# Performance work log

Hardware: AMD Instinct MI355X
Metric: run time of the kernel (lower is better)

The kernel has to match this reference:

```python
import jax, jax.numpy as jnp
import numpy as np

NB, NWAY, NBASE, FEAT, SEM = 8, 16, 8000, 512, 300
TEMP = float(np.sqrt(FEAT))  # d_k = feat_dim // n_head = 512


def setup_inputs() -> dict:
    key = jax.random.key(0)
    ks = jax.random.split(key, 18)
    n = jax.random.normal
    s_q = float(np.sqrt(2.0 / (FEAT + FEAT)))   # std for w_qs/w_ks/w_vs (d_model + d_k)
    s_sem = float(np.sqrt(2.0 / 600.0))
    s_lin = float(np.sqrt(1.0 / 300.0))
    return {
        "support_feat": n(ks[0], (NB, NWAY, FEAT), jnp.float32),
        "base_weights": n(ks[1], (NB, NBASE, FEAT), jnp.float32),
        "support_seman": n(ks[2], (NB, NWAY, SEM), jnp.float32),
        "base_seman": n(ks[3], (NB, NBASE, SEM), jnp.float32),
        # map_sem: Linear(300,300) -> LeakyReLU(0.1) -> Linear(300,300); weights stored (in,out)
        "map_w1": n(ks[4], (SEM, SEM), jnp.float32) * s_lin,
        "map_b1": jnp.zeros((SEM,), jnp.float32),
        "map_w2": n(ks[5], (SEM, SEM), jnp.float32) * s_lin,
        "map_b2": jnp.zeros((SEM,), jnp.float32),
        # task fusion gates: Linear(feat+300 -> feat) and Linear(feat+300 -> 300)
        "visfuse_w": n(ks[6], (FEAT + SEM, FEAT), jnp.float32) * s_lin,
        "visfuse_b": jnp.zeros((FEAT,), jnp.float32),
        "semfuse_w": n(ks[7], (FEAT + SEM, SEM), jnp.float32) * s_lin,
        "semfuse_b": jnp.zeros((SEM,), jnp.float32),
        # MHA projections (bias-free), stored (in,out)
        "w_qs": n(ks[8], (FEAT, FEAT), jnp.float32) * s_q,
        "w_ks": n(ks[9], (FEAT, FEAT), jnp.float32) * s_q,
        "w_vs": n(ks[10], (FEAT, FEAT), jnp.float32) * s_q,
        "w_qs_sem": n(ks[11], (SEM, FEAT), jnp.float32) * s_sem,
        "w_ks_sem": n(ks[12], (SEM, FEAT), jnp.float32) * s_sem,
        "fc_w": n(ks[13], (FEAT, FEAT), jnp.float32) * s_q,
    }


def _map_sem(x, w1, b1, w2, b2):
    return jax.nn.leaky_relu(x @ w1 + b1, negative_slope=0.1) @ w2 + b2


def _forward(support_feat, base_weights, support_seman, base_seman,
             map_w1, map_b1, map_w2, map_b2,
             visfuse_w, visfuse_b, semfuse_w, semfuse_b,
             w_qs, w_ks, w_vs, w_qs_sem, w_ks_sem, fc_w):
    # semantic calibration of both support and base semantics (base_seman_calib=True)
    support_seman = _map_sem(support_seman, map_w1, b1=map_b1, w2=map_w2, b2=map_b2)  # (nb,nway,300)
    base_seman = _map_sem(base_seman, map_w1, b1=map_b1, w2=map_w2, b2=map_b2)        # (nb,N,300)

    # avg_task_mem over base classes (repeat over nway is a no-op for the mean)
    avg = jnp.concatenate([jnp.mean(base_weights, axis=1, keepdims=True),
                           jnp.mean(base_seman, axis=1, keepdims=True)], axis=-1)      # (nb,1,feat+300)
    gate_vis = jax.nn.sigmoid(avg @ visfuse_w + visfuse_b) + 1.0                       # (nb,1,feat)
    gate_sem = jax.nn.sigmoid(avg @ semfuse_w + semfuse_b) + 1.0                       # (nb,1,300)

    base_mem_vis = base_weights                 # un-gated value memory (v)
    k_vis = base_weights * gate_vis             # gated keys
    k_sem = base_seman * gate_sem               # gated semantic keys

    # projections (n_head=1, d_k=d_v=feat)
    q = support_feat @ w_qs                     # (nb,nway,feat)
    k = k_vis @ w_ks                            # (nb,N,feat)
    v = base_mem_vis @ w_vs                     # (nb,N,feat)
    q_tot = q + support_seman @ w_qs_sem        # semantic-fused q
    k_tot = k + k_sem @ w_ks_sem                # semantic-fused k

    # each support sample attends over the shared base memory of its episode
    attn_score = jnp.einsum('bwd,bnd->bwn', q_tot, k_tot) / TEMP                       # (nb,nway,N)
    attn = jax.nn.softmax(attn_score, axis=-1)
    out = jnp.einsum('bwn,bnd->bwd', attn, v) @ fc_w + support_feat                    # residual
    # SupportCalibrator returns (support_center, support_attn=attn_score)
    return out, attn_score


def reference(support_feat, base_weights, support_seman, base_seman,
              map_w1, map_b1, map_w2, map_b2,
              visfuse_w, visfuse_b, semfuse_w, semfuse_b,
              w_qs, w_ks, w_vs, w_qs_sem, w_ks_sem, fc_w):
    return _forward(support_feat, base_weights, support_seman, base_seman,
                    map_w1, map_b1, map_w2, map_b2,
                    visfuse_w, visfuse_b, semfuse_w, semfuse_b,
                    w_qs, w_ks, w_vs, w_qs_sem, w_ks_sem, fc_w)
```

## Files before the change

### kernel.cpp

```cpp
#include <hip/hip_runtime.h>

#define NB 8
#define NWAY 16
#define NBASE 8000
#define FEAT 512
#define SEM 300
#define CAT (FEAT + SEM)
#define HLD 304

typedef __attribute__((ext_vector_type(8))) short bf16x8;
typedef __attribute__((ext_vector_type(4))) float f32x4;
typedef __attribute__((ext_vector_type(8))) unsigned short us8;
typedef __attribute__((ext_vector_type(4))) unsigned short us4;
typedef __attribute__((ext_vector_type(2))) unsigned short us2;
typedef unsigned short us;

__device__ __forceinline__ us f2bf(float x) {
    union { float f; unsigned int u; } v; v.f = x;
    unsigned int r = v.u + 0x7FFFu + ((v.u >> 16) & 1u);
    return (us)(r >> 16);
}
__device__ __forceinline__ float bf2f(us u) {
    union { unsigned int u; float f; } v; v.u = ((unsigned int)u) << 16;
    return v.f;
}

constexpr long O_BWH   = 0L;
constexpr long O_H     = 65536000L;
constexpr long O_W1T   = 104448000L;
constexpr long O_W2T   = 104652800L;
constexpr long O_QWT   = 104857600L;
constexpr long O_WVST  = 106496000L;
constexpr long O_FCWT  = 107020288L;
constexpr long O_PQT   = 107544576L;
constexpr long O_PMAX  = 107759616L;
constexpr long O_PSUM  = 107791872L;
constexpr long O_RMAX  = 107824128L;
constexpr long O_RINV  = 107824640L;
constexpr long O_F     = 107825152L;
constexpr long O_MBW   = O_F;
constexpr long O_MH    = O_F + 16384;
constexpr long O_GV    = O_F + 25984;
constexpr long O_GS    = O_F + 42368;
constexpr long O_SSMH  = O_F + 77952;
constexpr long O_QTG   = O_F + 77952;
constexpr long O_OV    = O_F + 233600;
constexpr long O_SFH   = O_F + 540800;
constexpr long O_PSG   = O_F + 540800;
constexpr long O_H1G   = O_F + 671872;
constexpr long O_CC    = O_F + 802944;
constexpr long O_WKST  = O_F + 803456;
constexpr long O_WKSST = O_F + 1327744;
constexpr long O_W2N   = O_F + 1655424;
constexpr long O_SSCG  = O_F + 1860224;

__global__ void k_prep(const float* __restrict__ w1, const float* __restrict__ w2,
                       const float* __restrict__ wqs, const float* __restrict__ wqss,
                       const float* __restrict__ wvs, const float* __restrict__ fcw,
                       const float* __restrict__ wks, const float* __restrict__ wkss,
                       const float* __restrict__ sf, const float* __restrict__ ssm,
                       us* __restrict__ w1t, us* __restrict__ w2t, us* __restrict__ qwT,
                       us* __restrict__ wvsT, us* __restrict__ fcwT,
                       us* __restrict__ wksT, us* __restrict__ wkssT, us* __restrict__ w2n,
                       us* __restrict__ sfh, us* __restrict__ ssmh,
                       float* __restrict__ mz, float* __restrict__ cz, us* __restrict__ pqt) {
    long e = (long)blockIdx.x * 256 + threadIdx.x;
    switch (blockIdx.y) {
    case 0: if (e < 320 * 320) { int n = e / 320, k = e % 320;
            w1t[e] = f2bf((n < SEM && k < SEM) ? w1[(long)k * SEM + n] : 0.f); } break;
    case 1: if (e < 320 * 320) { int n = e / 320, k = e % 320;
            w2t[e] = f2bf((n < SEM && k < SEM) ? w2[(long)k * SEM + n] : 0.f); } break;
    case 2: if (e < 512 * 832) { int n = e / 832, k = e % 832;
            float v = 0.f;
            if (k < FEAT) v = wqs[(long)k * FEAT + n];
            else if (k < CAT) v = wqss[(long)(k - FEAT) * FEAT + n];
            qwT[e] = f2bf(v); } break;
    case 3: if (e < 512 * 512) { int n = e / 512, k = e % 512;
            wvsT[e] = f2bf(wvs[(long)k * FEAT + n]); } break;
    case 4: if (e < 512 * 512) { int n = e / 512, k = e % 512;
            fcwT[e] = f2bf(fcw[(long)k * FEAT + n]); } break;
    case 5:
        if (e < NB * FEAT + NB * SEM) mz[e] = 0.f;
        if (e < NB * NWAY) cz[e] = 0.f;
        if (e < 128 * 28) pqt[(e / 28) * 840 + 812 + (e % 28)] = 0;
        break;
    case 6: if (e < 512 * 512) wksT[e] = f2bf(wks[e]); break;
    case 7: if (e < 320 * 512) { int n = e / 512, k = e % 512;
            wkssT[e] = (n < SEM) ? f2bf(wkss[(long)n * FEAT + k]) : (us)0; } break;
    case 8: if (e < 320 * 320) { int n = e / 320, k = e % 320;
            w2n[e] = (n < SEM && k < SEM) ? f2bf(w2[(long)n * SEM + k]) : (us)0; } break;
    case 9: if (e < 128 * 512) sfh[e] = f2bf(sf[e]); break;
    case 10: if (e < 128 * 320) { int n = e / 320, k = e % 320;
            ssmh[e] = (k < SEM) ? f2bf(ssm[(long)n * SEM + k]) : (us)0; } break;
    }
}

__global__ __launch_bounds__(256) void k_cvt_mlp1(
        const float* __restrict__ bw, us* __restrict__ bwh, float* __restrict__ mbw,
        const us* __restrict__ ssmh, const us* __restrict__ w1t,
        const float* __restrict__ b1, us* __restrict__ h1g) {
    __shared__ float red[128][4];
    const int bid = blockIdx.x;
    const int t = threadIdx.x;
    if (bid < 10) {
        const int ctile = bid % 5, rh = bid / 5;
        const int wv = t >> 6, lane = t & 63;
        const int m16 = lane & 15, q = lane >> 4;
        const int nc0 = ctile * 64;
        const int n = nc0 + wv * 16 + m16;
        f32x4 acc[4];
        #pragma unroll
        for (int i = 0; i < 4; ++i) acc[i] = (f32x4){0.f, 0.f, 0.f, 0.f};
        for (int ks = 0; ks < 10; ++ks) {
            const int k = ks * 32 + q * 8;
            bf16x8 bb = *(const bf16x8*)(w1t + (long)n * 320 + k);
            #pragma unroll
            for (int mt = 0; mt < 4; ++mt) {
                bf16x8 a = *(const bf16x8*)(ssmh + (long)(rh * 64 + mt * 16 + m16) * 320 + k);
                acc[mt] = __builtin_amdgcn_mfma_f32_16x16x32_bf16(a, bb, acc[mt], 0, 0, 0);
            }
        }
        const int col = n;
        const float bias = (col < SEM) ? b1[col] : 0.f;
        #pragma unroll
        for (int mt = 0; mt < 4; ++mt)
            #pragma unroll
            for (int r = 0; r < 4; ++r) {
                float v = acc[mt][r] + bias;
                v = v > 0.f ? v : 0.1f * v;
                const int gr = rh * 64 + mt * 16 + q * 4 + r;
                h1g[(long)gr * 320 + col] = (col < SEM) ? f2bf(v) : (us)0;
            }
        return;
    }
    const int fb = bid - 10;
    const int b = fb / 125, ch = fb % 125;
    int cg = t & 127, rs = t >> 7;
    long base = ((long)b * NBASE + (long)ch * 64) * FEAT + cg * 4;
    float s0 = 0.f, s1 = 0.f, s2 = 0.f, s3 = 0.f;
    for (int r0 = rs * 4; r0 < 64; r0 += 8) {
        float4 v[4];
        #pragma unroll
        for (int u = 0; u < 4; ++u)
            v[u] = *(const float4*)(bw + base + (long)(r0 + u) * FEAT);
        #pragma unroll
        for (int u = 0; u < 4; ++u) {
            us4 o; o.x = f2bf(v[u].x); o.y = f2bf(v[u].y); o.z = f2bf(v[u].z); o.w = f2bf(v[u].w);
            *(us4*)(bwh + base + (long)(r0 + u) * FEAT) = o;
            s0 += v[u].x; s1 += v[u].y; s2 += v[u].z; s3 += v[u].w;
        }
    }
    if (rs == 1) { red[cg][0] = s0; red[cg][1] = s1; red[cg][2] = s2; red[cg][3] = s3; }
    __syncthreads();
    if (rs == 0) {
        atomicAdd(&mbw[b * FEAT + cg * 4 + 0], s0 + red[cg][0]);
        atomicAdd(&mbw[b * FEAT + cg * 4 + 1], s1 + red[cg][1]);
        atomicAdd(&mbw[b * FEAT + cg * 4 + 2], s2 + red[cg][2]);
        atomicAdd(&mbw[b * FEAT + cg * 4 + 3], s3 + red[cg][3]);
    }
}

__global__ __launch_bounds__(256, 2) void k_hg_mlp2(const float* __restrict__ X,
        const us* __restrict__ W1T, const float* __restrict__ b1,
        us* __restrict__ H, float* __restrict__ mh,
        const us* __restrict__ h1g, const us* __restrict__ w2t,
        const float* __restrict__ b2, us* __restrict__ sscg) {
    __shared__ char smem[128 * 304 * 2];
    const int bid = blockIdx.x;
    const int t = threadIdx.x;
    const int wv = t >> 6, lane = t & 63;
    const int m16 = lane & 15, q = lane >> 4;
    if (bid < 10) {
        const int ctile = bid % 5, rh = bid / 5;
        const int n = ctile * 64 + wv * 16 + m16;
        f32x4 acc[4];
        #pragma unroll
        for (int i = 0; i < 4; ++i) acc[i] = (f32x4){0.f, 0.f, 0.f, 0.f};
        for (int ks = 0; ks < 10; ++ks) {
            const int k = ks * 32 + q * 8;
            bf16x8 bb = *(const bf16x8*)(w2t + (long)n * 320 + k);
            #pragma unroll
            for (int mt = 0; mt < 4; ++mt) {
                bf16x8 a = *(const bf16x8*)(h1g + (long)(rh * 64 + mt * 16 + m16) * 320 + k);
                acc[mt] = __builtin_amdgcn_mfma_f32_16x16x32_bf16(a, bb, acc[mt], 0, 0, 0);
            }
        }
        const int col = n;
        const float bias = (col < SEM) ? b2[col] : 0.f;
        #pragma unroll
        for (int mt = 0; mt < 4; ++mt)
            #pragma unroll
            for (int r = 0; r < 4; ++r) {
                const int gr = rh * 64 + mt * 16 + q * 4 + r;
                sscg[(long)gr * 320 + col] = (col < SEM) ? f2bf(acc[mt][r] + bias) : (us)0;
            }
        return;
    }
    us (*As)[72] = (us(*)[72])smem;
    us (*Bs)[72] = (us(*)[72])(smem + 18432);
    us (*Cs)[HLD] = (us(*)[HLD])smem;
    const int fb = bid - 10;
    const int b = fb / 63;
    const int bm = (fb % 63) * 128;
    const long rowbase = (long)b * NBASE;
    f32x4 acc[8][5];
    #pragma unroll
    for (int i = 0; i < 8; ++i)
        #pragma unroll
        for (int j = 0; j < 5; ++j) acc[i][j] = (f32x4){0.f, 0.f, 0.f, 0.f};
    for (int ks = 0; ks < 5; ++ks) {
        const int k0 = ks * 64;
        #pragma unroll
        for (int it = 0; it < 8; ++it) {
            int c = t + it * 256;
            int row = c >> 4, j = c & 15;
            int gk = k0 + j * 4;
            float4 v = make_float4(0.f, 0.f, 0.f, 0.f);
            if (gk < SEM && bm + row < NBASE)
                v = *(const float4*)(X + (rowbase + bm + row) * SEM + gk);
            us4 u; u.x = f2bf(v.x); u.y = f2bf(v.y); u.z = f2bf(v.z); u.w = f2bf(v.w);
            *(us4*)(&As[row][j * 4]) = u;
        }
        #pragma unroll
        for (int it = 0; it < 10; ++it) {
            int c = t + it * 256;
            int n = c >> 3, j = c & 7;
            int4 v = *(const int4*)(W1T + (long)n * 320 + k0 + j * 8);
            *(int4*)(&Bs[n][j * 8]) = v;
        }
        __syncthreads();
        #pragma unroll
        for (int kc = 0; kc < 64; kc += 32) {
            bf16x8 a[8], bb[5];
            #pragma unroll
            for (int rt = 0; rt < 8; ++rt)
                a[rt] = *(const bf16x8*)(&As[rt * 16 + m16][kc + q * 8]);
            #pragma unroll
            for (int ct = 0; ct < 5; ++ct)
                bb[ct] = *(const bf16x8*)(&Bs[(wv * 5 + ct) * 16 + m16][kc + q * 8]);
            #pragma unroll
            for (int rt = 0; rt < 8; ++rt)
                #pragma unroll
                for (int ct = 0; ct < 5; ++ct)
                    acc[rt][ct] = __builtin_amdgcn_mfma_f32_16x16x32_bf16(a[rt], bb[ct], acc[rt][ct], 0, 0, 0);
        }
        __syncthreads();
    }
    float csum[5] = {0.f, 0.f, 0.f, 0.f, 0.f};
    #pragma unroll
    for (int ct = 0; ct < 5; ++ct) {
        int col = (wv * 5 + ct) * 16 + m16;
        float bias = (col < SEM) ? b1[col] : 0.f;
        #pragma unroll
        for (int rt = 0; rt < 8; ++rt) {
            int rl = rt * 16 + q * 4;
            #pragma unroll
            for (int r = 0; r < 4; ++r) {
                float v = acc[rt][ct][r] + bias;
                v = v > 0.f ? v : 0.1f * v;
                if (col < SEM && bm + rl + r < NBASE) {
                    Cs[rl + r][col] = f2bf(v);
                    csum[ct] += v;
                }
            }
        }
    }
    if (t < 128) *(us4*)(&Cs[t][300]) = (us4){0, 0, 0, 0};
    #pragma unroll
    for (int ct = 0; ct < 5; ++ct) {
        float s = csum[ct];
        s += __shfl_xor(s, 16);
        s += __shfl_xor(s, 32);
        int col = (wv * 5 + ct) * 16 + m16;
        if (q == 0 && col < SEM) atomicAdd(&mh[b * SEM + col], s);
    }
    __syncthreads();
    for (int i = t; i < 128 * 76; i += 256) {
        int row = i / 76, j = i % 76;
        if (bm + row < NBASE)
            *(us4*)(H + (rowbase + bm + row) * HLD + j * 4) = *(const us4*)(&Cs[row][j * 4]);
    }
}

__global__ __launch_bounds__(256) void k_gates_qtot(
        const float* __restrict__ mbw, const float* __restrict__ mh,
        const float* __restrict__ mw2, const float* __restrict__ mb2,
        const float* __restrict__ vfw, const float* __restrict__ vfb,
        const float* __restrict__ sfw, const float* __restrict__ sfb,
        float* __restrict__ gv, float* __restrict__ gs,
        const us* __restrict__ sfh, const us* __restrict__ sscg,
        const us* __restrict__ qwT, us* __restrict__ qtotg) {
    __shared__ float avgL[CAT];
    __shared__ float mhL[SEM];
    __shared__ float red[4][64];
    const int bid = blockIdx.x;
    const int t = threadIdx.x;
    if (bid < 16) {
        const int ctile = bid % 8, rh = bid / 8;
        const int wv = t >> 6, lane = t & 63;
        const int m16 = lane & 15, q = lane >> 4;
        const int n = ctile * 64 + wv * 16 + m16;
        f32x4 acc[4];
        #pragma unroll
        for (int i = 0; i < 4; ++i) acc[i] = (f32x4){0.f, 0.f, 0.f, 0.f};
        for (int ks = 0; ks < 26; ++ks) {
            const int k = ks * 32 + q * 8;
            bf16x8 bb = *(const bf16x8*)(qwT + (long)n * 832 + k);
            #pragma unroll
            for (int mt = 0; mt < 4; ++mt) {
                const int gr = rh * 64 + mt * 16 + m16;
                bf16x8 a = (k < FEAT)
                    ? *(const bf16x8*)(sfh + (long)gr * 512 + k)
                    : *(const bf16x8*)(sscg + (long)gr * 320 + (k - FEAT));
                acc[mt] = __builtin_amdgcn_mfma_f32_16x16x32_bf16(a, bb, acc[mt], 0, 0, 0);
            }
        }
        #pragma unroll
        for (int mt = 0; mt < 4; ++mt)
            #pragma unroll
            for (int r = 0; r < 4; ++r) {
                const int gr = rh * 64 + mt * 16 + q * 4 + r;
                qtotg[(long)gr * 512 + n] = f2bf(acc[mt][r]);
            }
        return;
    }
    const int tile = (bid - 16) % 13, b = (bid - 16) / 13;
    const float invN = 1.0f / NBASE;
    for (int i = t; i < SEM; i += 256) mhL[i] = mh[b * SEM + i] * invN;
    for (int i = t; i < FEAT; i += 256) avgL[i] = mbw[b * FEAT + i] * invN;
    __syncthreads();
    for (int s = t; s < SEM; s += 256) {
        float a = mb2[s];
        for (int c = 0; c < SEM; ++c) a += mhL[c] * mw2[(long)c * SEM + s];
        avgL[FEAT + s] = a;
    }
    __syncthreads();
    int l = t & 63, kq = t >> 6;
    float a = 0.f;
    if (tile < 8) {
        int f = tile * 64 + l;
        for (int c = kq * 203; c < kq * 203 + 203; ++c) a += avgL[c] * vfw[(long)c * FEAT + f];
        red[kq][l] = a;
        __syncthreads();
        if (kq == 0) {
            float s = red[0][l] + red[1][l] + red[2][l] + red[3][l] + vfb[f];
            gv[b * FEAT + f] = 1.f + 1.f / (1.f + expf(-s));
        }
    } else {
        int fs = (tile - 8) * 64 + l;
        if (fs < SEM)
            for (int c = kq * 203; c < kq * 203 + 203; ++c) a += avgL[c] * sfw[(long)c * SEM + fs];
        red[kq][l] = a;
        __syncthreads();
        if (kq == 0 && fs < SEM) {
            float s = red[0][l] + red[1][l] + red[2][l] + red[3][l] + sfb[fs];
            gs[b * SEM + fs] = 1.f + 1.f / (1.f + expf(-s));
        }
    }
}

__global__ __launch_bounds__(256) void k_projgate(
        const us* __restrict__ qtotg, const us* __restrict__ wksT,
        const us* __restrict__ wkssT, const float* __restrict__ gv,
        const float* __restrict__ gs, const float* __restrict__ b2,
        us* __restrict__ pqt, us* __restrict__ psemG, float* __restrict__ cconst) {
    const int bid = blockIdx.x;
    const int nslot = bid % 13, rh = bid / 13;
    const int t = threadIdx.x;
    const int wv = t >> 6, lane = t & 63;
    const int m16 = lane & 15, q = lane >> 4;
    const bool isv = (nslot < 8);
    const int nc0 = isv ? nslot * 64 : (nslot - 8) * 64;
    const us* BT = isv ? wksT : wkssT;
    const int n = nc0 + wv * 16 + m16;
    f32x4 acc[4];
    #pragma unroll
    for (int i = 0; i < 4; ++i) acc[i] = (f32x4){0.f, 0.f, 0.f, 0.f};
    for (int ks = 0; ks < 16; ++ks) {
        const int k = ks * 32 + q * 8;
        bf16x8 bb = *(const bf16x8*)(BT + (long)n * 512 + k);
        #pragma unroll
        for (int mt = 0; mt < 4; ++mt) {
            bf16x8 a = *(const bf16x8*)(qtotg + (long)(rh * 64 + mt * 16 + m16) * 512 + k);
            acc[mt] = __builtin_amdgcn_mfma_f32_16x16x32_bf16(a, bb, acc[mt], 0, 0, 0);
        }
    }
    const int col = n;
    if (isv) {
        #pragma unroll
        for (int mt = 0; mt < 4; ++mt)
            #pragma unroll
            for (int r = 0; r < 4; ++r) {
                const int gr = rh * 64 + mt * 16 + q * 4 + r;
                const int b = gr >> 4;
                pqt[(long)gr * 840 + col] = f2bf(acc[mt][r] * gv[b * FEAT + col]);
            }
    } else {
        const float b2c = (col < SEM) ? b2[col] : 0.f;
        #pragma unroll
        for (int mt = 0; mt < 4; ++mt)
            #pragma unroll
            for (int r = 0; r < 4; ++r) {
                const int gr = rh * 64 + mt * 16 + q * 4 + r;
                const int b = gr >> 4;
                float p = (col < SEM) ? acc[mt][r] * gs[b * SEM + col] : 0.f;
                psemG[(long)gr * 320 + col] = (col < SEM) ? f2bf(p) : (us)0;
                float ps = p * b2c;
                ps += __shfl_xor(ps, 1); ps += __shfl_xor(ps, 2);
                ps += __shfl_xor(ps, 4); ps += __shfl_xor(ps, 8);
                if (m16 == 0) atomicAdd(&cconst[b * NWAY + (gr & 15)], ps);
            }
    }
}

__global__ __launch_bounds__(256) void k_sem2(const us* __restrict__ psemG,
        const us* __restrict__ w2n, us* __restrict__ pqt) {
    const int bid = blockIdx.x;
    const int ctile = bid % 5, rh = bid / 5;
    const int t = threadIdx.x;
    const int wv = t >> 6, lane = t & 63;
    const int m16 = lane & 15, q = lane >> 4;
    const int n = ctile * 64 + wv * 16 + m16;
    f32x4 acc[4];
    #pragma unroll
    for (int i = 0; i < 4; ++i) acc[i] = (f32x4){0.f, 0.f, 0.f, 0.f};
    for (int ks = 0; ks < 10; ++ks) {
        const int k = ks * 32 + q * 8;
        bf16x8 bb = *(const bf16x8*)(w2n + (long)n * 320 + k);
        #pragma unroll
        for (int mt = 0; mt < 4; ++mt) {
            bf16x8 a = *(const bf16x8*)(psemG + (long)(rh * 64 + mt * 16 + m16) * 320 + k);
            acc[mt] = __builtin_amdgcn_mfma_f32_16x16x32_bf16(a, bb, acc[mt], 0, 0, 0);
        }
    }
    const int col = n;
    if (col < SEM) {
        #pragma unroll
        for (int mt = 0; mt < 4; ++mt)
            #pragma unroll
            for (int r = 0; r < 4; ++r) {
                const int gr = rh * 64 + mt * 16 + q * 4 + r;
                pqt[(long)gr * 840 + 512 + col] = f2bf(acc[mt][r]);
            }
    }
}

__global__ __launch_bounds__(256) void k_scores_mfma(const us* __restrict__ bwh,
        const us* __restrict__ h, const us* __restrict__ pqt,
        const float* __restrict__ cconst, float* __restrict__ scores,
        float* __restrict__ pmax, float* __restrict__ psum) {
    __shared__ us As[128][72];
    __shared__ us Bs[NWAY][840];
    __shared__ float sred[4][16];
    const int b = blockIdx.y;
    const int bm = blockIdx.x * 128;
    const int t = threadIdx.x;
    const int wv = t >> 6, lane = t & 63;
    const int m16 = lane & 15, q = lane >> 4;
    for (int c = t; c < NWAY * 105; c += 256) {
        int n = c / 105, j = c % 105;
        *(int4*)(&Bs[n][j * 8]) = *(const int4*)(pqt + ((long)b * NWAY + n) * 840 + j * 8);
    }
    f32x4 acc[2];
    acc[0] = (f32x4){0, 0, 0, 0};
    acc[1] = (f32x4){0, 0, 0, 0};
    for (int ks = 0; ks < 13; ++ks) {
        int k0 = ks * 64;
        #pragma unroll
        for (int it = 0; it < 4; ++it) {
            int c = t + it * 256;
            int row = c >> 3, j = c & 7;
            int gm = bm + row, gk = k0 + j * 8;
            us8 u = (us8){0, 0, 0, 0, 0, 0, 0, 0};
            if (gk < FEAT)      u = *(const us8*)(bwh + ((long)b * NBASE + gm) * FEAT + gk);
            else if (gk < CAT)  u = *(const us8*)(h + ((long)b * NBASE + gm) * HLD + (gk - FEAT));
            *(us8*)(&As[row][j * 8]) = u;
        }
        __syncthreads();
        #pragma unroll
        for (int kc = 0; kc < 64; kc += 32) {
            bf16x8 bb = *(const bf16x8*)(&Bs[m16][k0 + kc + q * 8]);
            #pragma unroll
            for (int rt = 0; rt < 2; ++rt) {
                bf16x8 a = *(const bf16x8*)(&As[wv * 32 + rt * 16 + m16][kc + q * 8]);
                acc[rt] = __builtin_amdgcn_mfma_f32_16x16x32_bf16(a, bb, acc[rt], 0, 0, 0);
            }
        }
        __syncthreads();
    }
    const float invT = 0.04419417382415922f;
    float cadd = cconst[b * NWAY + m16];
    float vals[8];
    #pragma unroll
    for (int rt = 0; rt < 2; ++rt) {
        int nrow = bm + wv * 32 + rt * 16 + q * 4;
        #pragma unroll
        for (int r = 0; r < 4; ++r) {
            float v = (nrow + r < NBASE) ? (acc[rt][r] + cadd) * invT : -1e30f;
            vals[rt * 4 + r] = v;
        }
        if (nrow + 3 < NBASE) {
            float4 st = make_float4(vals[rt * 4], vals[rt * 4 + 1], vals[rt * 4 + 2], vals[rt * 4 + 3]);
            *(float4*)(scores + ((long)b * NWAY + m16) * NBASE + nrow) = st;
        } else {
            for (int r = 0; r < 4; ++r)
                if (nrow + r < NBASE)
                    scores[((long)b * NWAY + m16) * NBASE + nrow + r] = vals[rt * 4 + r];
        }
    }
    float lm = vals[0];
    #pragma unroll
    for (int i = 1; i < 8; ++i) lm = fmaxf(lm, vals[i]);
    lm = fmaxf(lm, __shfl_xor(lm, 16));
    lm = fmaxf(lm, __shfl_xor(lm, 32));
    if (q == 0) sred[wv][m16] = lm;
    __syncthreads();
    float bmax = fmaxf(fmaxf(sred[0][m16], sred[1][m16]), fmaxf(sred[2][m16], sred[3][m16]));
    __syncthreads();
    float ls = 0.f;
    #pragma unroll
    for (int i = 0; i < 8; ++i) ls += __expf(vals[i] - bmax);
    ls += __shfl_xor(ls, 16);
    ls += __shfl_xor(ls, 32);
    if (q == 0) sred[wv][m16] = ls;
    __syncthreads();
    if (wv == 0 && lane < 16) {
        float tot = sred[0][m16] + sred[1][m16] + sred[2][m16] + sred[3][m16];
        pmax[((long)b * NWAY + m16) * 63 + blockIdx.x] = bmax;
        psum[((long)b * NWAY + m16) * 63 + blockIdx.x] = tot;
    }
}

__global__ void k_combine(const float* __restrict__ pmax, const float* __restrict__ psum,
                          float* __restrict__ rmax, float* __restrict__ rinv,
                          float* __restrict__ ov) {
    int b = blockIdx.x, t = threadIdx.x;
    float4 z = make_float4(0.f, 0.f, 0.f, 0.f);
    for (int i = t; i < 2048; i += 256)
        *(float4*)(ov + ((long)b * 2048 + i) * 4) = z;
    int w = t >> 4, l = t & 15;
    long base = ((long)b * NWAY + w) * 63;
    float m = -1e30f;
    for (int i = l; i < 63; i += 16) m = fmaxf(m, pmax[base + i]);
    m = fmaxf(m, __shfl_xor(m, 1)); m = fmaxf(m, __shfl_xor(m, 2));
    m = fmaxf(m, __shfl_xor(m, 4)); m = fmaxf(m, __shfl_xor(m, 8));
    float s = 0.f;
    for (int i = l; i < 63; i += 16) s += psum[base + i] * __expf(pmax[base + i] - m);
    s += __shfl_xor(s, 1); s += __shfl_xor(s, 2);
    s += __shfl_xor(s, 4); s += __shfl_xor(s, 8);
    if (l == 0) { rmax[b * NWAY + w] = m; rinv[b * NWAY + w] = 1.0f / s; }
}

__global__ void k_ov(const float* __restrict__ scores, const float* __restrict__ rmax,
                     const float* __restrict__ rinv, const us* __restrict__ bwh,
                     float* __restrict__ ov) {
    int b = blockIdx.x, ch = blockIdx.y;
    int t = threadIdx.x;
    __shared__ float pr[NWAY][160];
    for (int i = t; i < NWAY * 160; i += 256) {
        int w = i / 160, j = i % 160;
        float sc = scores[((long)b * NWAY + w) * NBASE + (long)ch * 160 + j];
        pr[w][j] = __expf(sc - rmax[b * NWAY + w]) * rinv[b * NWAY + w];
    }
    __syncthreads();
    float a0[NWAY], a1[NWAY];
    #pragma unroll
    for (int w = 0; w < NWAY; ++w) { a0[w] = 0.f; a1[w] = 0.f; }
    const us* bp = bwh + ((long)b * NBASE + (long)ch * 160) * FEAT + 2 * t;
    for (int j0 = 0; j0 < 160; j0 += 8) {
        us2 u[8];
        #pragma unroll
        for (int uu = 0; uu < 8; ++uu)
            u[uu] = *(const us2*)(bp + (long)(j0 + uu) * FEAT);
        #pragma unroll
        for (int uu = 0; uu < 8; ++uu) {
            float v0 = bf2f(u[uu].x), v1 = bf2f(u[uu].y);
            #pragma unroll
            for (int w = 0; w < NWAY; ++w) {
                a0[w] += pr[w][j0 + uu] * v0;
                a1[w] += pr[w][j0 + uu] * v1;
            }
        }
    }
    for (int w = 0; w < NWAY; ++w) {
        atomicAdd(&ov[((long)b * NWAY + w) * FEAT + 2 * t], a0[w]);
        atomicAdd(&ov[((long)b * NWAY + w) * FEAT + 2 * t + 1], a1[w]);
    }
}

__global__ __launch_bounds__(256) void k_out(const float* __restrict__ ov,
        const us* __restrict__ wvsT, const us* __restrict__ fcwT,
        const float* __restrict__ sf, float* __restrict__ out) {
    __shared__ us Os[16][520];
    __shared__ us Ts[16][520];
    const int bx = blockIdx.x;
    const int t = threadIdx.x;
    const int wv = t >> 6, lane = t & 63;
    const int m16 = lane & 15, q = lane >> 4;
    const long r0 = (long)bx * NWAY;
    for (int i = t; i < 16 * 128; i += 256) {
        int r = i >> 7, c4 = (i & 127) * 4;
        float4 v = *(const float4*)(ov + (r0 + r) * FEAT + c4);
        us4 u; u.x = f2bf(v.x); u.y = f2bf(v.y); u.z = f2bf(v.z); u.w = f2bf(v.w);
        *(us4*)(&Os[r][c4]) = u;
    }
    __syncthreads();
    {
        f32x4 acc[8];
        #pragma unroll
        for (int i = 0; i < 8; ++i) acc[i] = (f32x4){0.f, 0.f, 0.f, 0.f};
        for (int ks = 0; ks < 16; ++ks) {
            bf16x8 a = *(const bf16x8*)(&Os[m16][ks * 32 + q * 8]);
            #pragma unroll
            for (int ct = 0; ct < 8; ++ct) {
                int nr = wv * 128 + ct * 16 + m16;
                bf16x8 bb = *(const bf16x8*)(wvsT + (long)nr * 512 + ks * 32 + q * 8);
                acc[ct] = __builtin_amdgcn_mfma_f32_16x16x32_bf16(a, bb, acc[ct], 0, 0, 0);
            }
        }
        #pragma unroll
        for (int ct = 0; ct < 8; ++ct) {
            int col = wv * 128 + ct * 16 + m16;
            #pragma unroll
            for (int r = 0; r < 4; ++r) Ts[q * 4 + r][col] = f2bf(acc[ct][r]);
        }
    }
    __syncthreads();
    {
        f32x4 acc[8];
        #pragma unroll
        for (int i = 0; i < 8; ++i) acc[i] = (f32x4){0.f, 0.f, 0.f, 0.f};
        for (int ks = 0; ks < 16; ++ks) {
            bf16x8 a = *(const bf16x8*)(&Ts[m16][ks * 32 + q * 8]);
            #pragma unroll
            for (int ct = 0; ct < 8; ++ct) {
                int nr = wv * 128 + ct * 16 + m16;
                bf16x8 bb = *(const bf16x8*)(fcwT + (long)nr * 512 + ks * 32 + q * 8);
                acc[ct] = __builtin_amdgcn_mfma_f32_16x16x32_bf16(a, bb, acc[ct], 0, 0, 0);
            }
        }
        #pragma unroll
        for (int ct = 0; ct < 8; ++ct) {
            int col = wv * 128 + ct * 16 + m16;
            #pragma unroll
            for (int r = 0; r < 4; ++r) {
                long row = r0 + q * 4 + r;
                out[row * FEAT + col] = acc[ct][r] + sf[row * FEAT + col];
            }
        }
    }
}

extern "C" void kernel_launch(void* const* d_in, const int* in_sizes, int n_in,
                              void* d_out, int out_size, void* d_ws, size_t ws_size,
                              hipStream_t stream) {
    (void)in_sizes; (void)n_in; (void)out_size; (void)ws_size;
    const float* sf   = (const float*)d_in[0];
    const float* bw   = (const float*)d_in[1];
    const float* ssm  = (const float*)d_in[2];
    const float* bsm  = (const float*)d_in[3];
    const float* mw1  = (const float*)d_in[4];
    const float* mb1  = (const float*)d_in[5];
    const float* mw2  = (const float*)d_in[6];
    const float* mb2  = (const float*)d_in[7];
    const float* vfw  = (const float*)d_in[8];
    const float* vfb  = (const float*)d_in[9];
    const float* sfw  = (const float*)d_in[10];
    const float* sfb  = (const float*)d_in[11];
    const float* wqs  = (const float*)d_in[12];
    const float* wks  = (const float*)d_in[13];
    const float* wvs  = (const float*)d_in[14];
    const float* wqss = (const float*)d_in[15];
    const float* wkss = (const float*)d_in[16];
    const float* fcw  = (const float*)d_in[17];

    float* out = (float*)d_out;
    float* scores = out + NB * NWAY * FEAT;

    char* wsb = (char*)d_ws;
    us* bwh    = (us*)(wsb + O_BWH);
    us* h      = (us*)(wsb + O_H);
    us* w1t    = (us*)(wsb + O_W1T);
    us* w2t    = (us*)(wsb + O_W2T);
    us* qwT    = (us*)(wsb + O_QWT);
    us* wvsT   = (us*)(wsb + O_WVST);
    us* fcwT   = (us*)(wsb + O_FCWT);
    us* pqt    = (us*)(wsb + O_PQT);
    us* wksT   = (us*)(wsb + O_WKST);
    us* wkssT  = (us*)(wsb + O_WKSST);
    us* w2n    = (us*)(wsb + O_W2N);
    us* sfh    = (us*)(wsb + O_SFH);
    us* ssmh   = (us*)(wsb + O_SSMH);
    us* h1g    = (us*)(wsb + O_H1G);
    us* sscg   = (us*)(wsb + O_SSCG);
    us* qtotg  = (us*)(wsb + O_QTG);
    us* psemG  = (us*)(wsb + O_PSG);
    float* pmax   = (float*)(wsb + O_PMAX);
    float* psum   = (float*)(wsb + O_PSUM);
    float* rmax   = (float*)(wsb + O_RMAX);
    float* rinv   = (float*)(wsb + O_RINV);
    float* mbw    = (float*)(wsb + O_MBW);
    float* mh     = (float*)(wsb + O_MH);
    float* gv     = (float*)(wsb + O_GV);
    float* gs     = (float*)(wsb + O_GS);
    float* ov     = (float*)(wsb + O_OV);
    float* cconst = (float*)(wsb + O_CC);

    k_prep<<<dim3(1664, 11), 256, 0, stream>>>(mw1, mw2, wqs, wqss, wvs, fcw, wks, wkss,
                                               sf, ssm,
                                               w1t, w2t, qwT, wvsT, fcwT, wksT, wkssT, w2n,
                                               sfh, ssmh, mbw, cconst, pqt);
    k_cvt_mlp1<<<1010, 256, 0, stream>>>(bw, bwh, mbw, ssmh, w1t, mb1, h1g);
    k_hg_mlp2<<<514, 256, 0, stream>>>(bsm, w1t, mb1, h, mh, h1g, w2t, mb2, sscg);
    k_gates_qtot<<<120, 256, 0, stream>>>(mbw, mh, mw2, mb2, vfw, vfb, sfw, sfb, gv, gs,
                                          sfh, sscg, qwT, qtotg);
    k_projgate<<<26, 256, 0, stream>>>(qtotg, wksT, wkssT, gv, gs, mb2, pqt, psemG, cconst);
    k_sem2<<<10, 256, 0, stream>>>(psemG, w2n, pqt);
    k_scores_mfma<<<dim3(63, NB), 256, 0, stream>>>(bwh, h, pqt, cconst, scores, pmax, psum);
    k_combine<<<NB, 256, 0, stream>>>(pmax, psum, rmax, rinv, ov);
    k_ov<<<dim3(NB, 50), 256, 0, stream>>>(scores, rmax, rinv, bwh, ov);
    k_out<<<NB, 256, 0, stream>>>(ov, wvsT, fcwT, sf, out);
}
```

Measured before the change: 569.0 us.

## Split output projection into two column-tiled MFMA kernels with workspace intermediate

```diff
diff --git a/kernel.cpp b/kernel.cpp
--- a/kernel.cpp
+++ b/kernel.cpp
@@ -588,67 +588,71 @@
     }
 }
 
-__global__ __launch_bounds__(256) void k_out(const float* __restrict__ ov,
-        const us* __restrict__ wvsT, const us* __restrict__ fcwT,
-        const float* __restrict__ sf, float* __restrict__ out) {
-    __shared__ us Os[16][520];
-    __shared__ us Ts[16][520];
-    const int bx = blockIdx.x;
+__global__ __launch_bounds__(256) void k_out1(const float* __restrict__ ov,
+        const us* __restrict__ wvsT, us* __restrict__ tmp) {
+    const int bid = blockIdx.x;
+    const int ctile = bid & 7, rh = bid >> 3;
     const int t = threadIdx.x;
     const int wv = t >> 6, lane = t & 63;
     const int m16 = lane & 15, q = lane >> 4;
-    const long r0 = (long)bx * NWAY;
-    for (int i = t; i < 16 * 128; i += 256) {
-        int r = i >> 7, c4 = (i & 127) * 4;
-        float4 v = *(const float4*)(ov + (r0 + r) * FEAT + c4);
-        us4 u; u.x = f2bf(v.x); u.y = f2bf(v.y); u.z = f2bf(v.z); u.w = f2bf(v.w);
-        *(us4*)(&Os[r][c4]) = u;
-    }
-    __syncthreads();
-    {
-        f32x4 acc[8];
-        #pragma unroll
-        for (int i = 0; i < 8; ++i) acc[i] = (f32x4){0.f, 0.f, 0.f, 0.f};
-        for (int ks = 0; ks < 16; ++ks) {
-            bf16x8 a = *(const bf16x8*)(&Os[m16][ks * 32 + q * 8]);
-            #pragma unroll
-            for (int ct = 0; ct < 8; ++ct) {
-                int nr = wv * 128 + ct * 16 + m16;
-                bf16x8 bb = *(const bf16x8*)(wvsT + (long)nr * 512 + ks * 32 + q * 8);
-                acc[ct] = __builtin_amdgcn_mfma_f32_16x16x32_bf16(a, bb, acc[ct], 0, 0, 0);
-            }
-        }
-        #pragma unroll
-        for (int ct = 0; ct < 8; ++ct) {
-            int col = wv * 128 + ct * 16 + m16;
-            #pragma unroll
-            for (int r = 0; r < 4; ++r) Ts[q * 4 + r][col] = f2bf(acc[ct][r]);
-        }
-    }
-    __syncthreads();
-    {
-        f32x4 acc[8];
-        #pragma unroll
-        for (int i = 0; i < 8; ++i) acc[i] = (f32x4){0.f, 0.f, 0.f, 0.f};
-        for (int ks = 0; ks < 16; ++ks) {
-            bf16x8 a = *(const bf16x8*)(&Ts[m16][ks * 32 + q * 8]);
-            #pragma unroll
-            for (int ct = 0; ct < 8; ++ct) {
-                int nr = wv * 128 + ct * 16 + m16;
-                bf16x8 bb = *(const bf16x8*)(fcwT + (long)nr * 512 + ks * 32 + q * 8);
-                acc[ct] = __builtin_amdgcn_mfma_f32_16x16x32_bf16(a, bb, acc[ct], 0, 0, 0);
-            }
-        }
-        #pragma unroll
-        for (int ct = 0; ct < 8; ++ct) {
-            int col = wv * 128 + ct * 16 + m16;
-            #pragma unroll
-            for (int r = 0; r < 4; ++r) {
-                long row = r0 + q * 4 + r;
-                out[row * FEAT + col] = acc[ct][r] + sf[row * FEAT + col];
-            }
-        }
-    }
+    const int n = ctile * 64 + wv * 16 + m16;
+    f32x4 acc[4];
+    #pragma unroll
+    for (int i = 0; i < 4; ++i) acc[i] = (f32x4){0.f, 0.f, 0.f, 0.f};
+    #pragma unroll 4
+    for (int ks = 0; ks < 16; ++ks) {
+        const int k = ks * 32 + q * 8;
+        bf16x8 bb = *(const bf16x8*)(wvsT + (long)n * 512 + k);
+        #pragma unroll
+        for (int mt = 0; mt < 4; ++mt) {
+            const float* ap = ov + (long)(rh * 64 + mt * 16 + m16) * 512 + k;
+            float4 x = *(const float4*)ap, y = *(const float4*)(ap + 4);
+            bf16x8 a;
+            a[0] = (short)f2bf(x.x); a[1] = (short)f2bf(x.y);
+            a[2] = (short)f2bf(x.z); a[3] = (short)f2bf(x.w);
+            a[4] = (short)f2bf(y.x); a[5] = (short)f2bf(y.y);
+            a[6] = (short)f2bf(y.z); a[7] = (short)f2bf(y.w);
+            acc[mt] = __builtin_amdgcn_mfma_f32_16x16x32_bf16(a, bb, acc[mt], 0, 0, 0);
+        }
+    }
+    #pragma unroll
+    for (int mt = 0; mt < 4; ++mt)
+        #pragma unroll
+        for (int r = 0; r < 4; ++r) {
+            const int gr = rh * 64 + mt * 16 + q * 4 + r;
+            tmp[(long)gr * 512 + n] = f2bf(acc[mt][r]);
+        }
+}
+
+__global__ __launch_bounds__(256) void k_out2(const us* __restrict__ tmp,
+        const us* __restrict__ fcwT, const float* __restrict__ sf,
+        float* __restrict__ out) {
+    const int bid = blockIdx.x;
+    const int ctile = bid & 7, rh = bid >> 3;
+    const int t = threadIdx.x;
+    const int wv = t >> 6, lane = t & 63;
+    const int m16 = lane & 15, q = lane >> 4;
+    const int n = ctile * 64 + wv * 16 + m16;
+    f32x4 acc[4];
+    #pragma unroll
+    for (int i = 0; i < 4; ++i) acc[i] = (f32x4){0.f, 0.f, 0.f, 0.f};
+    #pragma unroll 4
+    for (int ks = 0; ks < 16; ++ks) {
+        const int k = ks * 32 + q * 8;
+        bf16x8 bb = *(const bf16x8*)(fcwT + (long)n * 512 + k);
+        #pragma unroll
+        for (int mt = 0; mt < 4; ++mt) {
+            bf16x8 a = *(const bf16x8*)(tmp + (long)(rh * 64 + mt * 16 + m16) * 512 + k);
+            acc[mt] = __builtin_amdgcn_mfma_f32_16x16x32_bf16(a, bb, acc[mt], 0, 0, 0);
+        }
+    }
+    #pragma unroll
+    for (int mt = 0; mt < 4; ++mt)
+        #pragma unroll
+        for (int r = 0; r < 4; ++r) {
+            const long gr = rh * 64 + mt * 16 + q * 4 + r;
+            out[gr * FEAT + n] = acc[mt][r] + sf[gr * FEAT + n];
+        }
 }
 
 extern "C" void kernel_launch(void* const* d_in, const int* in_sizes, int n_in,
@@ -719,5 +723,6 @@
     k_scores_mfma<<<dim3(63, NB), 256, 0, stream>>>(bwh, h, pqt, cconst, scores, pmax, psum);
     k_combine<<<NB, 256, 0, stream>>>(pmax, psum, rmax, rinv, ov);
     k_ov<<<dim3(NB, 50), 256, 0, stream>>>(scores, rmax, rinv, bwh, ov);
-    k_out<<<NB, 256, 0, stream>>>(ov, wvsT, fcwT, sf, out);
-}
+    k_out1<<<16, 256, 0, stream>>>(ov, wvsT, qtotg);
+    k_out2<<<16, 256, 0, stream>>>(qtotg, fcwT, sf, out);
+}
```

Measured after the change: 522.2 us. -8.2%, faster.
